# Kernel tuning notes

Measured on AMD Instinct MI355X. Metric: run time of the kernel, lower is better.

## Reference

```python
import jax, jax.numpy as jnp
import numpy as np

B, S, D = 2, 2048, 2048
N_HEADS, N_KV_HEADS = 16, 4
HEAD_DIM = D // N_HEADS


def setup_inputs() -> dict:
    key = jax.random.key(0)
    ks = jax.random.split(key, 5)
    x = jax.random.normal(ks[0], (B, S, D), dtype=jnp.float32)
    W_q = jax.random.normal(ks[1], (D, D), dtype=jnp.float32) * 0.02
    W_k = jax.random.normal(ks[2], (D, N_KV_HEADS * HEAD_DIM), dtype=jnp.float32) * 0.02
    W_v = jax.random.normal(ks[3], (D, N_KV_HEADS * HEAD_DIM), dtype=jnp.float32) * 0.02
    W_o = jax.random.normal(ks[4], (D, D), dtype=jnp.float32) * 0.02
    return {"x": x, "W_q": W_q, "W_k": W_k, "W_v": W_v, "W_o": W_o}


def _apply_rope(xh, positions):
    # xh: [B, H, S, Dh]; rotate adjacent pairs as complex numbers
    Dh = xh.shape[-1]
    half = Dh // 2
    freqs = 1.0 / (10000.0 ** (jnp.arange(half, dtype=jnp.float32) / half))  # [half]
    angles = positions[:, None].astype(jnp.float32) * freqs[None, :]          # [S, half]
    cos, sin = jnp.cos(angles), jnp.sin(angles)
    xp = xh.reshape(*xh.shape[:-1], half, 2)
    x0, x1 = xp[..., 0], xp[..., 1]
    r0 = x0 * cos - x1 * sin
    r1 = x0 * sin + x1 * cos
    return jnp.stack([r0, r1], axis=-1).reshape(xh.shape)


def reference(x, W_q, W_k, W_v, W_o):
    b, s, d = x.shape
    positions = jnp.arange(s)
    rep = N_HEADS // N_KV_HEADS
    Q = (x @ W_q).reshape(b, s, N_HEADS, HEAD_DIM).transpose(0, 2, 1, 3)        # [B,H,S,Dh]
    K = (x @ W_k).reshape(b, s, N_KV_HEADS, HEAD_DIM).transpose(0, 2, 1, 3)     # [B,Hkv,S,Dh]
    V = (x @ W_v).reshape(b, s, N_KV_HEADS, HEAD_DIM).transpose(0, 2, 1, 3)
    Qr = _apply_rope(Q, positions)
    # torch .repeat(1, rep, 1, 1) tiles kv-head blocks: head h -> kv head h % n_kv_heads
    K_rep = jnp.tile(K, (1, rep, 1, 1))
    V_rep = jnp.tile(V, (1, rep, 1, 1))
    Kr = _apply_rope(K_rep, positions)
    scores = jnp.einsum('bhqd,bhkd->bhqk', Qr, Kr) / (HEAD_DIM ** 0.5)
    weights = jax.nn.softmax(scores, axis=-1)
    out = jnp.einsum('bhqk,bhkd->bhqd', weights, V_rep)
    out = out.transpose(0, 2, 1, 3).reshape(b, s, d)
    return out @ W_o
```

## Files before the change

### kernel.cpp

```cpp
#include <hip/hip_runtime.h>


typedef __attribute__((ext_vector_type(8))) short  short8;
typedef __attribute__((ext_vector_type(8))) __bf16 bf16x8;
typedef __attribute__((ext_vector_type(4))) float  f32x4;

#define B_   2
#define S_   2048
#define D_   2048
#define H_   16
#define HKV_ 4
#define DH_  128
#define M_   4096
#define NQKV 3072

static __device__ __forceinline__ ushort f2bf(float f) {
  __bf16 h = (__bf16)f;
  return __builtin_bit_cast(unsigned short, h);
}
static __device__ __forceinline__ float bf2f(ushort u) {
  union { unsigned u; float f; } v; v.u = ((unsigned)u) << 16;
  return v.f;
}
static __device__ __forceinline__ f32x4 mfma16(short8 a, short8 b, f32x4 c) {
  return __builtin_amdgcn_mfma_f32_16x16x32_bf16(
      __builtin_bit_cast(bf16x8, a), __builtin_bit_cast(bf16x8, b), c, 0, 0, 0);
}
static __device__ __forceinline__ void gload16(const ushort* g, ushort* l) {
  __builtin_amdgcn_global_load_lds(
      (const __attribute__((address_space(1))) unsigned int*)g,
      (__attribute__((address_space(3))) unsigned int*)l, 16, 0, 0);
}
template <int N>
static __device__ __forceinline__ void vmwait() {
  asm volatile("s_waitcnt vmcnt(%0)" :: "n"(N) : "memory");
}

__global__ __launch_bounds__(256) void prep(const float* __restrict__ x,
                                            const float* __restrict__ Wq,
                                            const float* __restrict__ Wk,
                                            const float* __restrict__ Wv,
                                            const float* __restrict__ Wo,
                                            ushort* __restrict__ xb,
                                            ushort* __restrict__ Wqkvt,
                                            ushort* __restrict__ Wot,
                                            float2* __restrict__ tab) {
  __shared__ float tile[32][33];
  const int b = blockIdx.x, tid = threadIdx.x;
  if (b < 8192) {
    int i = b * 256 + tid;
    float4 v = ((const float4*)x)[i];
    ushort4 o;
    o.x = f2bf(v.x); o.y = f2bf(v.y); o.z = f2bf(v.z); o.w = f2bf(v.w);
    ((ushort4*)xb)[i] = o;
    return;
  }
  if (b < 8704) {
    int i = (b - 8704 + 512) * 256 + tid;
    int pos = i >> 6, f = i & 63;
    float freq = powf(10000.0f, -(float)f / 64.0f);
    float a = (float)pos * freq;
    tab[i] = make_float2(cosf(a), sinf(a));
    return;
  }
  int t = b - 8704;
  const float* src; ushort* dst; int R, C, bx, by;
  if (t < 4096)      { src = Wq; dst = Wqkvt;                        R = 2048; C = 2048; bx = t & 63; by = t >> 6; }
  else if (t < 5120) { t -= 4096; src = Wk; dst = Wqkvt + (size_t)2048 * 2048; R = 2048; C = 512;  bx = t & 15; by = t >> 4; }
  else if (t < 6144) { t -= 5120; src = Wv; dst = Wqkvt + (size_t)2560 * 2048; R = 2048; C = 512;  bx = t & 15; by = t >> 4; }
  else               { t -= 6144; src = Wo; dst = Wot;                R = 2048; C = 2048; bx = t & 63; by = t >> 6; }
  int c0 = bx * 32, r0 = by * 32;
  int tx = tid & 31, ty = tid >> 5;
#pragma unroll
  for (int i = 0; i < 32; i += 8)
    tile[ty + i][tx] = src[(size_t)(r0 + ty + i) * C + c0 + tx];
  __syncthreads();
#pragma unroll
  for (int i = 0; i < 32; i += 8)
    dst[(size_t)(c0 + ty + i) * R + r0 + tx] = f2bf(tile[tx][ty + i]);
}

__global__ void transpose_v(const ushort* __restrict__ in,
                            ushort* __restrict__ out, int src_stride) {
  __shared__ ushort tile[32][33];
  int bkv = blockIdx.z;
  const ushort* src = in + (size_t)(bkv >> 2) * S_ * src_stride + (bkv & 3) * DH_;
  ushort* dst = out + (size_t)bkv * DH_ * S_;
  int d0 = blockIdx.x * 32, s0 = blockIdx.y * 32;
  int tx = threadIdx.x, ty = threadIdx.y;
#pragma unroll
  for (int i = 0; i < 32; i += 8)
    tile[ty + i][tx] = src[(size_t)(s0 + ty + i) * src_stride + d0 + tx];
  __syncthreads();
#pragma unroll
  for (int i = 0; i < 32; i += 8)
    dst[(size_t)(d0 + ty + i) * S_ + s0 + tx] = tile[tx][ty + i];
}

__global__ void rope_both(ushort* __restrict__ qkv,
                          const float2* __restrict__ tab, float qscale) {
  int idx = blockIdx.x * blockDim.x + threadIdx.x;
  const int total_q = M_ * 1024;
  ushort* t; int ppr_shift; float oscale;
  if (idx < total_q) { t = qkv; ppr_shift = 10; oscale = qscale; }
  else { idx -= total_q; t = qkv + 2048; ppr_shift = 8; oscale = 1.0f; }
  int row = idx >> ppr_shift;
  int p   = idx & ((1 << ppr_shift) - 1);
  int head = p >> 6, fi = p & 63;
  int pos = row & (S_ - 1);
  float2 cs = tab[(pos << 6) + fi];
  size_t off = (size_t)row * NQKV + head * DH_ + 2 * fi;
  ushort2 v = *(ushort2*)&t[off];
  float x0 = bf2f(v.x), x1 = bf2f(v.y);
  ushort2 o;
  o.x = f2bf((x0 * cs.x - x1 * cs.y) * oscale);
  o.y = f2bf((x0 * cs.y + x1 * cs.x) * oscale);
  *(ushort2*)&t[off] = o;
}

template <int BN, int NF, typename OutT>
__global__ __launch_bounds__(512, 1) void gemm4p(const ushort* __restrict__ A,
                                                 const ushort* __restrict__ Bt,
                                                 OutT* __restrict__ C,
                                                 int M, int N, int K) {
  __shared__ ushort As[2][256 * 64];
  __shared__ ushort Bs[2][BN * 64];
  constexpr int NBR = BN / 64;
  const int tid = threadIdx.x;
  const int lane = tid & 63, w = tid >> 6;
  const int l16 = lane & 15, l4 = lane >> 4;
  const int wm = (w >> 1) * 64, wn = (w & 1) * (BN / 2);
  const int bm = blockIdx.x * 256, bn = blockIdx.y * BN;
  const int swz = l16 & 7;

  const ushort* gA = A  + (size_t)bm * K;
  const ushort* gB = Bt + (size_t)bn * K;
  const int srow = tid >> 3;
  const int scb  = tid & 7;
  const int sswz = srow & 7;

  auto stageA = [&](int t, int s, int g) {
    int row = g * 64 + srow;
    gload16(gA + (size_t)row * K + t * 64 + ((scb ^ sswz) * 8),
            &As[s][(g * 64 + w * 8) * 64]);
  };
  auto stageA4 = [&](int t, int s) {
#pragma unroll
    for (int g = 0; g < 4; ++g) stageA(t, s, g);
  };
  auto stageBall = [&](int t, int s) {
#pragma unroll
    for (int g = 0; g < NBR; ++g) {
      int row = g * 64 + srow;
      gload16(gB + (size_t)row * K + t * 64 + ((scb ^ sswz) * 8),
              &Bs[s][(g * 64 + w * 8) * 64]);
    }
  };

  f32x4 acc[4][NF] = {};
  short8 bfr[NF][2];
  const int NT  = K / 64;
  const int NIT = K / 128;

  stageBall(0, 0);
  stageA4(0, 0);
  stageBall(1, 1);
  vmwait<NBR>();
  __builtin_amdgcn_s_barrier();
  __builtin_amdgcn_sched_barrier(0);

#define GPHASE(S, J, ISSUES, VMW)                                             \
  {                                                                           \
    short8 afr[2][2];                                                         \
    _Pragma("unroll")                                                         \
    for (int mf = 0; mf < 2; ++mf) {                                          \
      _Pragma("unroll")                                                       \
      for (int kk = 0; kk < 2; ++kk) {                                        \
        int row = wm + (J) * 32 + mf * 16 + l16;                              \
        afr[mf][kk] =                                                         \
            *(const short8*)&As[S][row * 64 + (((kk * 4 + l4) ^ swz) * 8)];   \
      }                                                                       \
    }                                                                         \
    if ((J) == 0) {                                                           \
      _Pragma("unroll")                                                       \
      for (int nf = 0; nf < NF; ++nf) {                                       \
        _Pragma("unroll")                                                     \
        for (int kk = 0; kk < 2; ++kk) {                                      \
          int row = wn + nf * 16 + l16;                                       \
          bfr[nf][kk] =                                                       \
              *(const short8*)&Bs[S][row * 64 + (((kk * 4 + l4) ^ swz) * 8)]; \
        }                                                                     \
      }                                                                       \
    }                                                                         \
    ISSUES;                                                                   \
    __builtin_amdgcn_s_barrier();                                             \
    asm volatile("s_waitcnt lgkmcnt(0)" ::: "memory");                        \
    __builtin_amdgcn_sched_barrier(0);                                        \
    __builtin_amdgcn_s_setprio(1);                                            \
    _Pragma("unroll")                                                         \
    for (int kk = 0; kk < 2; ++kk) {                                          \
      _Pragma("unroll")                                                       \
      for (int mf = 0; mf < 2; ++mf) {                                        \
        _Pragma("unroll")                                                     \
        for (int nf = 0; nf < NF; ++nf)                                       \
          acc[(J) * 2 + mf][nf] =                                             \
              mfma16(afr[mf][kk], bfr[nf][kk], acc[(J) * 2 + mf][nf]);        \
      }                                                                       \
    }                                                                         \
    __builtin_amdgcn_s_setprio(0);                                            \
    VMW;                                                                      \
    __builtin_amdgcn_s_barrier();                                             \
    __builtin_amdgcn_sched_barrier(0);                                        \
  }

  for (int i = 0; i < NIT; ++i) {
    const int tb = 2 * i + 1;
    const int t2 = (2 * i + 2 < NT) ? 2 * i + 2 : NT - 1;
    const int t3 = (2 * i + 3 < NT) ? 2 * i + 3 : NT - 1;
    GPHASE(0, 0, (stageA4(tb, 1)),  (void)0)
    GPHASE(0, 1, (stageBall(t2, 0)), vmwait<NBR>())
    GPHASE(1, 0, (stageA4(t2, 0)),  (void)0)
    GPHASE(1, 1, (stageBall(t3, 1)), vmwait<NBR>())
  }
#undef GPHASE

  asm volatile("s_waitcnt vmcnt(0)" ::: "memory");

#pragma unroll
  for (int mi = 0; mi < 4; ++mi) {
#pragma unroll
    for (int nf = 0; nf < NF; ++nf) {
#pragma unroll
      for (int r = 0; r < 4; ++r) {
        size_t row = bm + wm + (mi >> 1) * 32 + (mi & 1) * 16 + l4 * 4 + r;
        size_t col = bn + wn + nf * 16 + l16;
        if constexpr (sizeof(OutT) == 2)
          C[row * N + col] = f2bf(acc[mi][nf][r]);
        else
          C[row * N + col] = acc[mi][nf][r];
      }
    }
  }
}

__global__ __launch_bounds__(256, 2) void flash_attn(const ushort* __restrict__ Qp,
                                                     const ushort* __restrict__ Kp,
                                                     const ushort* __restrict__ Vt,
                                                     ushort* __restrict__ Oa) {
  __shared__ ushort Ks[2][64 * 128];
  __shared__ ushort Vs[2][128 * 64];
  const int tid = threadIdx.x;
  const int lane = tid & 63, wave = tid >> 6;
  const int l16 = lane & 15, l4 = lane >> 4;
  const int bh = blockIdx.y;
  const int b = bh >> 4, h = bh & 15, kv = h & 3;
  const int q0 = blockIdx.x * 128 + wave * 32;

  short8 qf[2][4];
#pragma unroll
  for (int qg = 0; qg < 2; ++qg) {
    const ushort* qrow =
        Qp + ((size_t)(b * S_ + q0 + qg * 16 + l16)) * NQKV + h * DH_ + l4 * 8;
#pragma unroll
    for (int kk = 0; kk < 4; ++kk) qf[qg][kk] = *(const short8*)(qrow + kk * 32);
  }

  const ushort* kbase = Kp + (size_t)(b * S_) * NQKV + kv * DH_;
  const ushort* vbase = Vt + (size_t)(b * HKV_ + kv) * DH_ * S_;

  float mreg[2] = {-1e30f, -1e30f};
  f32x4 o[2][8] = {};
  f32x4 ol[2] = {};
  short8 onesf;
#pragma unroll
  for (int j = 0; j < 8; ++j) onesf[j] = (short)0x3F80;

  const int kswz = (l16 & 3) | (((l16 >> 2) & 1) << 2);
  const int vswz = l16 & 7;

  const int krT = wave * 16 + (lane >> 4);
  const int kcT = lane & 15;
  const int vrT = wave * 32 + (lane >> 3);
  const int vcT = lane & 7;

  auto stage = [&](int t, int buf) {
#pragma unroll
    for (int i = 0; i < 4; ++i) {
      int r = krT + i * 4;
      int swzk = (r & 3) | (((r >> 3) & 1) << 2);
      gload16(kbase + (size_t)(t * 64 + r) * NQKV + ((kcT ^ swzk) * 8),
              &Ks[buf][(wave * 16 + i * 4) * 128]);
      int d = vrT + i * 8;
      gload16(vbase + (size_t)d * S_ + t * 64 + ((vcT ^ (d & 7)) * 8),
              &Vs[buf][(wave * 32 + i * 8) * 64]);
    }
  };

  const int NT = S_ / 64;
  stage(0, 0);
  __syncthreads();

  for (int t = 0; t < NT; ++t) {
    const int cur = t & 1;
    if (t + 1 < NT) stage(t + 1, cur ^ 1);

    f32x4 s[2][4] = {};
    __builtin_amdgcn_s_setprio(1);
#pragma unroll
    for (int c = 0; c < 4; ++c) {
      const int krow = 32 * (c >> 1) + 8 * (l16 >> 2) + 4 * (c & 1) + (l16 & 3);
#pragma unroll
      for (int kk = 0; kk < 4; ++kk) {
        short8 kf = *(const short8*)&Ks[cur][krow * 128 + (((kk * 4 + l4) ^ kswz) * 8)];
        s[0][c] = mfma16(kf, qf[0][kk], s[0][c]);
        s[1][c] = mfma16(kf, qf[1][kk], s[1][c]);
      }
    }
    __builtin_amdgcn_s_setprio(0);

    float lmax[2];
#pragma unroll
    for (int qg = 0; qg < 2; ++qg) {
      float a = fmaxf(fmaxf(s[qg][0][0], s[qg][0][1]), fmaxf(s[qg][0][2], s[qg][0][3]));
#pragma unroll
      for (int c = 1; c < 4; ++c) {
        a = fmaxf(a, fmaxf(fmaxf(s[qg][c][0], s[qg][c][1]),
                           fmaxf(s[qg][c][2], s[qg][c][3])));
      }
      lmax[qg] = a;
    }

    bool ok = (lmax[0] - mreg[0] <= 8.0f) && (lmax[1] - mreg[1] <= 8.0f);
    if (!__all(ok)) {
#pragma unroll
      for (int qg = 0; qg < 2; ++qg) {
        float a = fmaxf(lmax[qg], __shfl_xor(lmax[qg], 16));
        float tmax = fmaxf(a, __shfl_xor(a, 32));
        float mn = fmaxf(mreg[qg], tmax);
        float alpha = __builtin_amdgcn_exp2f(mreg[qg] - mn);
        mreg[qg] = mn;
        float af[4];
#pragma unroll
        for (int r = 0; r < 4; ++r)
          af[r] = __shfl(alpha, (lane & 48) + l4 * 4 + r);
#pragma unroll
        for (int g = 0; g < 8; ++g)
#pragma unroll
          for (int r = 0; r < 4; ++r) o[qg][g][r] *= af[r];
#pragma unroll
        for (int r = 0; r < 4; ++r) ol[qg][r] *= af[r];
      }
    }

    short8 pa[2];
#pragma unroll
    for (int ks = 0; ks < 2; ++ks) {
#pragma unroll
      for (int qg = 0; qg < 2; ++qg) {
        short8 pk;
#pragma unroll
        for (int j = 0; j < 8; ++j) {
          float p = __builtin_amdgcn_exp2f(s[qg][2 * ks + (j >> 2)][j & 3] - mreg[qg]);
          pk[j] = (short)f2bf(p);
        }
        pa[qg] = pk;
      }
      __builtin_amdgcn_s_setprio(1);
#pragma unroll
      for (int g = 0; g < 8; ++g) {
        const int d = g * 16 + l16;
        short8 vf = *(const short8*)&Vs[cur][d * 64 + (((ks * 4 + l4) ^ vswz) * 8)];
        o[0][g] = mfma16(pa[0], vf, o[0][g]);
        o[1][g] = mfma16(pa[1], vf, o[1][g]);
      }
      ol[0] = mfma16(pa[0], onesf, ol[0]);
      ol[1] = mfma16(pa[1], onesf, ol[1]);
      __builtin_amdgcn_s_setprio(0);
    }

    __syncthreads();
  }

#pragma unroll
  for (int qg = 0; qg < 2; ++qg) {
    float invq[4];
#pragma unroll
    for (int r = 0; r < 4; ++r) invq[r] = 1.0f / ol[qg][r];
    ushort* op = Oa + (size_t)(b * S_ + q0 + qg * 16) * D_ + h * DH_;
#pragma unroll
    for (int g = 0; g < 8; ++g)
#pragma unroll
      for (int r = 0; r < 4; ++r)
        op[(size_t)(l4 * 4 + r) * D_ + g * 16 + l16] = f2bf(o[qg][g][r] * invq[r]);
  }
}

extern "C" void kernel_launch(void* const* d_in, const int* in_sizes, int n_in,
                              void* d_out, int out_size, void* d_ws, size_t ws_size,
                              hipStream_t stream) {
  (void)in_sizes; (void)n_in; (void)out_size; (void)ws_size;
  const float* x  = (const float*)d_in[0];
  const float* Wq = (const float*)d_in[1];
  const float* Wk = (const float*)d_in[2];
  const float* Wv = (const float*)d_in[3];
  const float* Wo = (const float*)d_in[4];
  float* out = (float*)d_out;

  size_t off = 0;
  auto carve = [&](size_t bytes) -> void* {
    void* p = (char*)d_ws + off;
    off += (bytes + 255) & ~(size_t)255;
    return p;
  };
  ushort* xb    = (ushort*)carve((size_t)M_ * D_ * 2);
  ushort* Wqkvt = (ushort*)carve((size_t)NQKV * D_ * 2);
  ushort* Wot   = (ushort*)carve((size_t)D_ * D_ * 2);
  ushort* QKV   = (ushort*)carve((size_t)M_ * NQKV * 2);
  ushort* Vt    = (ushort*)carve((size_t)M_ * 512 * 2);
  ushort* attn  = (ushort*)carve((size_t)M_ * D_ * 2);
  float2* tab   = (float2*)carve((size_t)S_ * 64 * sizeof(float2));

  prep<<<18944, 256, 0, stream>>>(x, Wq, Wk, Wv, Wo, xb, Wqkvt, Wot, tab);

  gemm4p<192, 6, ushort><<<dim3(16, 16), 512, 0, stream>>>(xb, Wqkvt, QKV, M_, NQKV, 2048);

  const float qscale = 0.08838834764831845f * 1.4426950408889634f;
  rope_both<<<(M_ * 1280) / 256, 256, 0, stream>>>(QKV, tab, qscale);
  transpose_v<<<dim3(4, 64, 8), dim3(32, 8), 0, stream>>>(QKV + 2560, Vt, NQKV);

  flash_attn<<<dim3(S_ / 128, B_ * H_), 256, 0, stream>>>(QKV, QKV + 2048, Vt, attn);

  gemm4p<128, 4, float><<<dim3(16, 16), 512, 0, stream>>>(attn, Wot, out, M_, 2048, 2048);
}
```

Before: 198.5 us.

## Use triple-buffered 32-key tiles with vmcnt-based waits in flash attention

The flash attention loop now stages 32-key K/V tiles into a three-slot LDS ring, prefetching two tiles ahead. It waits on outstanding vector-memory counts plus a single barrier per tile instead of a full __syncthreads at the end of each iteration. The aim is to hide global-load latency better and cut synchronisation stalls. The cost is twice as many loop iterations and twice as many softmax rescale checks. The running max now starts at 0 instead of -1e30, which depends on the lazy-rescale threshold bounding overflow.

After: 207.1 us. +4.3%, slower.

```diff
diff --git a/kernel.cpp b/kernel.cpp
--- a/kernel.cpp
+++ b/kernel.cpp
@@ -247,8 +247,8 @@
                                                      const ushort* __restrict__ Kp,
                                                      const ushort* __restrict__ Vt,
                                                      ushort* __restrict__ Oa) {
-  __shared__ ushort Ks[2][64 * 128];
-  __shared__ ushort Vs[2][128 * 64];
+  __shared__ ushort Ks[3][32 * 128];
+  __shared__ ushort Vs[3][128 * 32];
   const int tid = threadIdx.x;
   const int lane = tid & 63, wave = tid >> 6;
   const int l16 = lane & 15, l4 = lane >> 4;
@@ -268,7 +268,7 @@
   const ushort* kbase = Kp + (size_t)(b * S_) * NQKV + kv * DH_;
   const ushort* vbase = Vt + (size_t)(b * HKV_ + kv) * DH_ * S_;
 
-  float mreg[2] = {-1e30f, -1e30f};
+  float mreg[2] = {0.f, 0.f};
   f32x4 o[2][8] = {};
   f32x4 ol[2] = {};
   short8 onesf;
@@ -276,42 +276,45 @@
   for (int j = 0; j < 8; ++j) onesf[j] = (short)0x3F80;
 
   const int kswz = (l16 & 3) | (((l16 >> 2) & 1) << 2);
-  const int vswz = l16 & 7;
-
-  const int krT = wave * 16 + (lane >> 4);
-  const int kcT = lane & 15;
-  const int vrT = wave * 32 + (lane >> 3);
-  const int vcT = lane & 7;
-
-  auto stage = [&](int t, int buf) {
-#pragma unroll
-    for (int i = 0; i < 4; ++i) {
-      int r = krT + i * 4;
+
+  const int krT = tid >> 4;
+  const int kcT = tid & 15;
+  const int vrT = tid >> 2;
+  const int vcT = tid & 3;
+
+  auto stage = [&](int t, int s) {
+#pragma unroll
+    for (int i = 0; i < 2; ++i) {
+      int r = i * 16 + krT;
       int swzk = (r & 3) | (((r >> 3) & 1) << 2);
-      gload16(kbase + (size_t)(t * 64 + r) * NQKV + ((kcT ^ swzk) * 8),
-              &Ks[buf][(wave * 16 + i * 4) * 128]);
-      int d = vrT + i * 8;
-      gload16(vbase + (size_t)d * S_ + t * 64 + ((vcT ^ (d & 7)) * 8),
-              &Vs[buf][(wave * 32 + i * 8) * 64]);
+      gload16(kbase + (size_t)(t * 32 + r) * NQKV + ((kcT ^ swzk) * 8),
+              &Ks[s][(i * 16 + wave * 4) * 128]);
+      int d = i * 64 + vrT;
+      gload16(vbase + (size_t)d * S_ + t * 32 + ((vcT ^ (d & 3)) * 8),
+              &Vs[s][(i * 64 + wave * 16) * 32]);
     }
   };
 
-  const int NT = S_ / 64;
+  const int NT = S_ / 32;
+  vmwait<0>();
   stage(0, 0);
-  __syncthreads();
+  stage(1, 1);
+  int sc = 0, sn = 1, sx = 2;
 
   for (int t = 0; t < NT; ++t) {
-    const int cur = t & 1;
-    if (t + 1 < NT) stage(t + 1, cur ^ 1);
-
-    f32x4 s[2][4] = {};
+    if (t < NT - 1) vmwait<4>(); else vmwait<0>();
+    __builtin_amdgcn_s_barrier();
+    __builtin_amdgcn_sched_barrier(0);
+    if (t + 2 < NT) stage(t + 2, sx);
+
+    f32x4 s[2][2] = {};
     __builtin_amdgcn_s_setprio(1);
 #pragma unroll
-    for (int c = 0; c < 4; ++c) {
-      const int krow = 32 * (c >> 1) + 8 * (l16 >> 2) + 4 * (c & 1) + (l16 & 3);
+    for (int c = 0; c < 2; ++c) {
+      const int krow = 8 * (l16 >> 2) + 4 * c + (l16 & 3);
 #pragma unroll
       for (int kk = 0; kk < 4; ++kk) {
-        short8 kf = *(const short8*)&Ks[cur][krow * 128 + (((kk * 4 + l4) ^ kswz) * 8)];
+        short8 kf = *(const short8*)&Ks[sc][krow * 128 + (((kk * 4 + l4) ^ kswz) * 8)];
         s[0][c] = mfma16(kf, qf[0][kk], s[0][c]);
         s[1][c] = mfma16(kf, qf[1][kk], s[1][c]);
       }
@@ -321,12 +324,10 @@
     float lmax[2];
 #pragma unroll
     for (int qg = 0; qg < 2; ++qg) {
-      float a = fmaxf(fmaxf(s[qg][0][0], s[qg][0][1]), fmaxf(s[qg][0][2], s[qg][0][3]));
-#pragma unroll
-      for (int c = 1; c < 4; ++c) {
-        a = fmaxf(a, fmaxf(fmaxf(s[qg][c][0], s[qg][c][1]),
-                           fmaxf(s[qg][c][2], s[qg][c][3])));
-      }
+      float a = fmaxf(fmaxf(s[qg][0][0], s[qg][0][1]),
+                      fmaxf(s[qg][0][2], s[qg][0][3]));
+      a = fmaxf(a, fmaxf(fmaxf(s[qg][1][0], s[qg][1][1]),
+                         fmaxf(s[qg][1][2], s[qg][1][3])));
       lmax[qg] = a;
     }
 
@@ -354,31 +355,29 @@
 
     short8 pa[2];
 #pragma unroll
-    for (int ks = 0; ks < 2; ++ks) {
-#pragma unroll
-      for (int qg = 0; qg < 2; ++qg) {
-        short8 pk;
-#pragma unroll
-        for (int j = 0; j < 8; ++j) {
-          float p = __builtin_amdgcn_exp2f(s[qg][2 * ks + (j >> 2)][j & 3] - mreg[qg]);
-          pk[j] = (short)f2bf(p);
-        }
-        pa[qg] = pk;
+    for (int qg = 0; qg < 2; ++qg) {
+      short8 pk;
+#pragma unroll
+      for (int j = 0; j < 8; ++j) {
+        float p = __builtin_amdgcn_exp2f(s[qg][j >> 2][j & 3] - mreg[qg]);
+        pk[j] = (short)f2bf(p);
       }
-      __builtin_amdgcn_s_setprio(1);
-#pragma unroll
-      for (int g = 0; g < 8; ++g) {
-        const int d = g * 16 + l16;
-        short8 vf = *(const short8*)&Vs[cur][d * 64 + (((ks * 4 + l4) ^ vswz) * 8)];
-        o[0][g] = mfma16(pa[0], vf, o[0][g]);
-        o[1][g] = mfma16(pa[1], vf, o[1][g]);
-      }
-      ol[0] = mfma16(pa[0], onesf, ol[0]);
-      ol[1] = mfma16(pa[1], onesf, ol[1]);
-      __builtin_amdgcn_s_setprio(0);
-    }
-
-    __syncthreads();
+      pa[qg] = pk;
+    }
+
+    __builtin_amdgcn_s_setprio(1);
+#pragma unroll
+    for (int g = 0; g < 8; ++g) {
+      const int d = g * 16 + l16;
+      short8 vf = *(const short8*)&Vs[sc][d * 32 + ((l4 ^ (d & 3)) * 8)];
+      o[0][g] = mfma16(pa[0], vf, o[0][g]);
+      o[1][g] = mfma16(pa[1], vf, o[1][g]);
+    }
+    ol[0] = mfma16(pa[0], onesf, ol[0]);
+    ol[1] = mfma16(pa[1], onesf, ol[1]);
+    __builtin_amdgcn_s_setprio(0);
+
+    int tmp = sc; sc = sn; sn = sx; sx = tmp;
   }
 
 #pragma unroll
```
